# Performance work log

Hardware: AMD Instinct MI355X
Metric: run time of the kernel (lower is better)

Reference implementation:

```python
import jax, jax.numpy as jnp
import numpy as np

N_NODES = 50000
N_EDGES = 1600000
IN_C, HID_C, OUT_C = 256, 256, 10


def setup_inputs() -> dict:
    key = jax.random.key(0)
    ks = jax.random.split(key, 8)
    x = jax.random.normal(ks[0], (N_NODES, IN_C), dtype=jnp.float32)
    edge_index = jax.random.randint(ks[1], (2, N_EDGES), 0, N_NODES, dtype=jnp.int64)
    s1 = 1.0 / np.sqrt(IN_C)
    s2 = 1.0 / np.sqrt(HID_C)
    W1l = jax.random.normal(ks[2], (IN_C, HID_C), dtype=jnp.float32) * s1
    W1r = jax.random.normal(ks[3], (IN_C, HID_C), dtype=jnp.float32) * s1
    b1 = jnp.zeros((HID_C,), dtype=jnp.float32)
    W2l = jax.random.normal(ks[4], (HID_C, OUT_C), dtype=jnp.float32) * s2
    W2r = jax.random.normal(ks[5], (HID_C, OUT_C), dtype=jnp.float32) * s2
    b2 = jnp.zeros((OUT_C,), dtype=jnp.float32)
    return {"x": x, "edge_index": edge_index, "W1l": W1l, "W1r": W1r,
            "b1": b1, "W2l": W2l, "W2r": W2r, "b2": b2}


def _mean_agg(x, src, dst, n):
    # scatter-mean of source features into destination nodes
    summed = jax.ops.segment_sum(x[src], dst, num_segments=n)  # [N, C]
    cnt = jax.ops.segment_sum(jnp.ones_like(dst, dtype=x.dtype), dst, num_segments=n)
    return summed / jnp.maximum(cnt, 1.0)[:, None]


def _sage_conv(x, src, dst, Wl, Wr, b):
    # PyG SAGEConv (mean aggr): lin_l(mean_j x_j) + lin_r(x_i) + bias
    n = x.shape[0]
    agg = _mean_agg(x, src, dst, n)
    return agg @ Wl + x @ Wr + b


def reference(x, edge_index, W1l, W1r, b1, W2l, W2r, b2):
    src = edge_index[0]
    dst = edge_index[1]
    h = _sage_conv(x, src, dst, W1l, W1r, b1)
    h = jax.nn.relu(h)  # dropout skipped: eval mode
    out = _sage_conv(h, src, dst, W2l, W2r, b2)
    return jax.nn.log_softmax(out, axis=1)
```

## Files before the change

kernel.cpp:

```cpp
#include <hip/hip_runtime.h>
#include <hip/hip_bf16.h>

#define N_NODES 50000
#define N_EDGES 1600000
#define IN_C 256
#define HID_C 256
#define OUT_C 10
#define SLOT_CAP 96
#define NBUCKET 196
#define EBUF_CAP 9216
#define M_TILES 391
#define PART_BLOCKS 391
#define PREP_BLOCKS 532

typedef short bf16x8 __attribute__((ext_vector_type(8)));
typedef float f32x4 __attribute__((ext_vector_type(4)));

static __device__ __forceinline__ float b2f(short v) {
    unsigned u = (unsigned)(unsigned short)v << 16;
    return __builtin_bit_cast(float, u);
}
static __device__ __forceinline__ short f2b(float f) {
    __hip_bfloat16 h = __float2bfloat16(f);
    return __builtin_bit_cast(short, h);
}
static __device__ __forceinline__ int4 pack8i(float4 a, float4 b) {
    bf16x8 o;
    o[0] = f2b(a.x); o[1] = f2b(a.y); o[2] = f2b(a.z); o[3] = f2b(a.w);
    o[4] = f2b(b.x); o[5] = f2b(b.y); o[6] = f2b(b.z); o[7] = f2b(b.w);
    return __builtin_bit_cast(int4, o);
}

__global__ __launch_bounds__(256) void k_pp(
        const float* __restrict__ W1l, const float* __restrict__ W1r,
        const float* __restrict__ W2l, const float* __restrict__ W2r,
        __hip_bfloat16* __restrict__ Wt, float* __restrict__ Wt2f,
        const int* __restrict__ src, const int* __restrict__ dst,
        int* __restrict__ g_cursor, int* __restrict__ ebuf) {
    __shared__ int pbuf[3 * 256];
    int tid = threadIdx.x;
    int bid = blockIdx.x;

    if (bid < 512) {
        int idx = bid * 256 + tid;
        int n = idx >> 8, k = idx & 255;
        float v = (n < HID_C) ? W1l[k * HID_C + n] : W1r[k * HID_C + (n - HID_C)];
        Wt[idx] = __float2bfloat16(v);
        return;
    }
    if (bid < PREP_BLOCKS) {
        int idx = (bid - 512) * 256 + tid;
        int r = idx >> 8, k = idx & 255;
        if (r < OUT_C) Wt2f[r * 256 + k] = W2l[k * OUT_C + r];
        else           Wt2f[(16 + r - OUT_C) * 256 + k] = W2r[k * OUT_C + (r - OUT_C)];
        return;
    }

    int* hist = pbuf;
    int* base = pbuf + 256;
    int* pos  = pbuf + 512;
    int pb = bid - PREP_BLOCKS;
    if (tid < NBUCKET) { hist[tid] = 0; pos[tid] = 0; }
    __syncthreads();

    int4 s[4], d[4];
    bool valid[4];
#pragma unroll
    for (int q = 0; q < 4; ++q) {
        int idx = pb * 1024 + q * 256 + tid;
        valid[q] = (idx < N_EDGES / 4);
        if (valid[q]) {
            s[q] = ((const int4*)src)[idx];
            d[q] = ((const int4*)dst)[idx];
        }
    }
#pragma unroll
    for (int q = 0; q < 4; ++q) {
        if (valid[q]) {
            atomicAdd(&hist[d[q].x >> 8], 1);
            atomicAdd(&hist[d[q].y >> 8], 1);
            atomicAdd(&hist[d[q].z >> 8], 1);
            atomicAdd(&hist[d[q].w >> 8], 1);
        }
    }
    __syncthreads();
    if (tid < NBUCKET && hist[tid] > 0)
        base[tid] = atomicAdd(&g_cursor[tid], hist[tid]);
    __syncthreads();
#pragma unroll
    for (int q = 0; q < 4; ++q) {
        if (valid[q]) {
            int ss[4] = { s[q].x, s[q].y, s[q].z, s[q].w };
            int dd[4] = { d[q].x, d[q].y, d[q].z, d[q].w };
#pragma unroll
            for (int e = 0; e < 4; ++e) {
                int b = dd[e] >> 8;
                int p = base[b] + atomicAdd(&pos[b], 1);
                if (p < EBUF_CAP)
                    ebuf[b * EBUF_CAP + p] = ss[e] | ((dd[e] & 255) << 16);
            }
        }
    }
}

__global__ __launch_bounds__(256) void k_gb(
        const int* __restrict__ ebuf, const int* __restrict__ g_cursor,
        int* __restrict__ cnt, unsigned short* __restrict__ slots,
        const float* __restrict__ X, const __hip_bfloat16* __restrict__ Wt,
        const float* __restrict__ b1,
        __hip_bfloat16* __restrict__ Ab, __hip_bfloat16* __restrict__ Bh) {
    __shared__ short Smem[2 * 128 * 64];
    int tid = threadIdx.x;

    if (blockIdx.x < NBUCKET) {
        int* lcnt = (int*)Smem;
        int b = blockIdx.x;
        lcnt[tid] = 0;
        __syncthreads();
        int n_e = g_cursor[b];
        if (n_e > EBUF_CAP) n_e = EBUF_CAP;
        const int* eb = ebuf + b * EBUF_CAP;
        int n4 = n_e >> 2;
        for (int t = tid; t < n4; t += 256) {
            int4 v = ((const int4*)eb)[t];
            int vv[4] = { v.x, v.y, v.z, v.w };
#pragma unroll
            for (int e = 0; e < 4; ++e) {
                int dl = (vv[e] >> 16) & 255;
                int sv = vv[e] & 0xFFFF;
                int p = atomicAdd(&lcnt[dl], 1);
                if (p < SLOT_CAP) slots[(size_t)(b * 256 + dl) * SLOT_CAP + p] = (unsigned short)sv;
            }
        }
        for (int t = (n4 << 2) + tid; t < n_e; t += 256) {
            int vv = eb[t];
            int dl = (vv >> 16) & 255;
            int sv = vv & 0xFFFF;
            int p = atomicAdd(&lcnt[dl], 1);
            if (p < SLOT_CAP) slots[(size_t)(b * 256 + dl) * SLOT_CAP + p] = (unsigned short)sv;
        }
        __syncthreads();
        int nid = b * 256 + tid;
        if (nid < N_NODES) cnt[nid] = lcnt[tid];
        return;
    }

    short* As = Smem;
    short* Bs = Smem + 128 * 64;
    int fid = blockIdx.x - NBUCKET;
    int xcd = fid & 7, slot = fid >> 3;
    int m_t = (slot >> 2) * 8 + xcd;
    if (m_t >= M_TILES) return;
    int n_t = slot & 3;
    int m_base = m_t * 128;
    int n_base = n_t * 128;

    int wave = tid >> 6, lane = tid & 63;
    int r = lane & 15, quad = lane >> 4;
    int wr = wave >> 1, wc = wave & 1;

    int srow = tid >> 3;
    int kb8  = (tid & 7) * 16;
    int kelem = (tid & 7) * 8;
    int swz  = kb8 ^ ((srow & 7) << 4);

    f32x4 acc[4][4];
#pragma unroll
    for (int i = 0; i < 4; ++i)
#pragma unroll
        for (int j = 0; j < 4; ++j) acc[i][j] = f32x4{0.f, 0.f, 0.f, 0.f};

    int4 av[4], bv[4];
#pragma unroll
    for (int q = 0; q < 4; ++q) {
        int grow = m_base + q * 32 + srow;
        if (grow > N_NODES - 1) grow = N_NODES - 1;
        const float* xp = X + (size_t)grow * IN_C + kelem;
        av[q] = pack8i(*(const float4*)xp, *(const float4*)(xp + 4));
        int brow = n_base + q * 32 + srow;
        bv[q] = *(const int4*)((const char*)Wt + ((size_t)brow * 512 + kb8));
    }

    for (int kk = 0; kk < 4; ++kk) {
        if (kk) __syncthreads();
#pragma unroll
        for (int q = 0; q < 4; ++q) {
            *(int4*)((char*)As + (size_t)((q * 32 + srow) * 128 + swz)) = av[q];
            *(int4*)((char*)Bs + (size_t)((q * 32 + srow) * 128 + swz)) = bv[q];
        }
        __syncthreads();

        if (kk < 3) {
            int ke = (kk + 1) * 64 + kelem;
            int kbyte = (kk + 1) * 128 + kb8;
#pragma unroll
            for (int q = 0; q < 4; ++q) {
                int grow = m_base + q * 32 + srow;
                if (grow > N_NODES - 1) grow = N_NODES - 1;
                const float* xp = X + (size_t)grow * IN_C + ke;
                av[q] = pack8i(*(const float4*)xp, *(const float4*)(xp + 4));
                int brow = n_base + q * 32 + srow;
                bv[q] = *(const int4*)((const char*)Wt + ((size_t)brow * 512 + kbyte));
            }
        }

#pragma unroll
        for (int s = 0; s < 2; ++s) {
            int kfb = (s * 64 + quad * 16) ^ ((r & 7) << 4);
            bf16x8 a[4], b[4];
#pragma unroll
            for (int i = 0; i < 4; ++i)
                a[i] = *(const bf16x8*)((const char*)As + (size_t)((wr * 64 + i * 16 + r) * 128) + kfb);
#pragma unroll
            for (int j = 0; j < 4; ++j)
                b[j] = *(const bf16x8*)((const char*)Bs + (size_t)((wc * 64 + j * 16 + r) * 128) + kfb);
#pragma unroll
            for (int i = 0; i < 4; ++i)
#pragma unroll
                for (int j = 0; j < 4; ++j)
                    acc[i][j] = __builtin_amdgcn_mfma_f32_16x16x32_bf16(a[i], b[j], acc[i][j], 0, 0, 0);
        }
    }

    __syncthreads();
    short* Cs = Smem;
    bool left = (n_base < HID_C);
#pragma unroll
    for (int j = 0; j < 4; ++j) {
        int coll = wc * 64 + 16 * j + r;
        float bias = left ? 0.f : b1[n_base + coll - HID_C];
#pragma unroll
        for (int i = 0; i < 4; ++i) {
#pragma unroll
            for (int ii = 0; ii < 4; ++ii) {
                int rowl = wr * 64 + 16 * i + quad * 4 + ii;
                int byteoff = (coll * 2) ^ ((rowl & 7) << 4);
                *(short*)((char*)Cs + rowl * 256 + byteoff) = f2b(acc[i][j][ii] + bias);
            }
        }
    }
    __syncthreads();

    int rrow = tid >> 4;
    int cchunk = (tid & 15) * 16;
    size_t colbyte = left ? (size_t)(n_base * 2) : (size_t)((n_base - HID_C) * 2);
    char* outp = left ? (char*)Ab : (char*)Bh;
    for (int rb = 0; rb < 128; rb += 16) {
        int rowl = rb + rrow;
        int4 v = *(const int4*)((const char*)Cs + rowl * 256 + (cchunk ^ ((rowl & 7) << 4)));
        int grow = m_base + rowl;
        if (grow < N_NODES)
            *(int4*)(outp + (size_t)grow * 512 + colbyte + cchunk) = v;
    }
}

__global__ __launch_bounds__(256) void k_agg1f(
        const __hip_bfloat16* __restrict__ Ab, const __hip_bfloat16* __restrict__ Bh,
        const int* __restrict__ cnt, const unsigned short* __restrict__ slots,
        const float* __restrict__ Wt2f, const float* __restrict__ b2,
        float* __restrict__ CDl, float* __restrict__ CDr) {
    int wave = threadIdx.x >> 6, lane = threadIdx.x & 63;
    int nid = blockIdx.x * 4 + wave;
    int half = lane >> 5;
    int c8 = (lane & 31) * 8;
    const unsigned short* row = slots + (size_t)nid * SLOT_CAP;
    int n = cnt[nid];
    if (n > SLOT_CAP) n = SLOT_CAP;
    int mid = (n + 1) >> 1;
    int beg = half ? mid : 0;
    int end = half ? n : mid;

    float s0[8], s1[8], s2[8], s3[8];
#pragma unroll
    for (int j = 0; j < 8; ++j) { s0[j] = 0.f; s1[j] = 0.f; s2[j] = 0.f; s3[j] = 0.f; }

    const __hip_bfloat16* abc = Ab + c8;
    int e = beg;
    for (; e + 4 <= end; e += 4) {
        int i0 = row[e], i1 = row[e + 1], i2 = row[e + 2], i3 = row[e + 3];
        bf16x8 v0 = *(const bf16x8*)(abc + (size_t)i0 * HID_C);
        bf16x8 v1 = *(const bf16x8*)(abc + (size_t)i1 * HID_C);
        bf16x8 v2 = *(const bf16x8*)(abc + (size_t)i2 * HID_C);
        bf16x8 v3 = *(const bf16x8*)(abc + (size_t)i3 * HID_C);
#pragma unroll
        for (int j = 0; j < 8; ++j) {
            s0[j] += b2f(v0[j]); s1[j] += b2f(v1[j]);
            s2[j] += b2f(v2[j]); s3[j] += b2f(v3[j]);
        }
    }
    for (; e < end; ++e) {
        int i0 = row[e];
        bf16x8 v0 = *(const bf16x8*)(abc + (size_t)i0 * HID_C);
#pragma unroll
        for (int j = 0; j < 8; ++j) s0[j] += b2f(v0[j]);
    }
#pragma unroll
    for (int j = 0; j < 8; ++j) s0[j] += (s1[j] + s2[j]) + s3[j];
#pragma unroll
    for (int j = 0; j < 8; ++j) s0[j] += __shfl_down(s0[j], 32, 64);

    float h[8];
    float inv = 1.f / fmaxf((float)n, 1.f);
    if (half == 0) {
        bf16x8 bb = *(const bf16x8*)(Bh + (size_t)nid * HID_C + c8);
#pragma unroll
        for (int j = 0; j < 8; ++j)
            h[j] = fmaxf(s0[j] * inv + b2f(bb[j]), 0.f);
    }
#pragma unroll
    for (int j = 0; j < 8; ++j) h[j] = __shfl(h[j], lane & 31, 64);

    const float* wbase = Wt2f + (half ? 16 * 256 : 0);
    float acc[10];
#pragma unroll
    for (int j = 0; j < 10; ++j) {
        f32x4 w0 = *(const f32x4*)(wbase + j * 256 + c8);
        f32x4 w1 = *(const f32x4*)(wbase + j * 256 + c8 + 4);
        float a = h[0] * w0[0] + h[1] * w0[1] + h[2] * w0[2] + h[3] * w0[3]
                + h[4] * w1[0] + h[5] * w1[1] + h[6] * w1[2] + h[7] * w1[3];
#pragma unroll
        for (int off = 16; off > 0; off >>= 1)
            a += __shfl_down(a, off, 32);
        acc[j] = a;
    }
    if ((lane & 31) == 0) {
        if (half == 0) {
            float* o = CDl + (size_t)nid * 12;
#pragma unroll
            for (int j = 0; j < 10; ++j) o[j] = acc[j];
            o[10] = 0.f; o[11] = 0.f;
        } else {
            float* o = CDr + (size_t)nid * 12;
#pragma unroll
            for (int j = 0; j < 10; ++j) o[j] = acc[j] + b2[j];
        }
    }
}

__global__ __launch_bounds__(256) void k_agg2(
        const float* __restrict__ CDl, const float* __restrict__ CDr,
        const int* __restrict__ cnt, const unsigned short* __restrict__ slots,
        float* __restrict__ out) {
    int wave = threadIdx.x >> 6, lane = threadIdx.x & 63;
    int half = lane >> 5, sub = lane & 31;
    int nid = blockIdx.x * 8 + wave * 2 + half;
    const unsigned short* row = slots + (size_t)nid * SLOT_CAP;
    int n = cnt[nid];
    if (n > SLOT_CAP) n = SLOT_CAP;
    float s[10];
#pragma unroll
    for (int j = 0; j < 10; ++j) s[j] = 0.f;
    for (int e = sub; e < n; e += 32) {
        const float* cr = CDl + (size_t)row[e] * 12;
        f32x4 v0 = *(const f32x4*)cr;
        f32x4 v1 = *(const f32x4*)(cr + 4);
        f32x4 v2 = *(const f32x4*)(cr + 8);
#pragma unroll
        for (int j = 0; j < 4; ++j) { s[j] += v0[j]; s[4 + j] += v1[j]; }
        s[8] += v2[0]; s[9] += v2[1];
    }
#pragma unroll
    for (int j = 0; j < 10; ++j)
#pragma unroll
        for (int off = 16; off > 0; off >>= 1)
            s[j] += __shfl_down(s[j], off, 32);
    if (sub == 0) {
        float inv = 1.f / fmaxf((float)n, 1.f);
        const float* rr = CDr + (size_t)nid * 12;
        float z[10], mx = -1e30f;
#pragma unroll
        for (int j = 0; j < 10; ++j) {
            z[j] = s[j] * inv + rr[j];
            mx = fmaxf(mx, z[j]);
        }
        float se = 0.f;
#pragma unroll
        for (int j = 0; j < 10; ++j) se += expf(z[j] - mx);
        float lse = logf(se) + mx;
#pragma unroll
        for (int j = 0; j < 10; ++j) out[(size_t)nid * OUT_C + j] = z[j] - lse;
    }
}

extern "C" void kernel_launch(void* const* d_in, const int* in_sizes, int n_in,
                              void* d_out, int out_size, void* d_ws, size_t ws_size,
                              hipStream_t stream) {
    const float* x   = (const float*)d_in[0];
    const int*   ei  = (const int*)d_in[1];
    const float* W1l = (const float*)d_in[2];
    const float* W1r = (const float*)d_in[3];
    const float* b1  = (const float*)d_in[4];
    const float* W2l = (const float*)d_in[5];
    const float* W2r = (const float*)d_in[6];
    const float* b2  = (const float*)d_in[7];
    float* out = (float*)d_out;
    const int* src = ei;
    const int* dst = ei + N_EDGES;

    char* w = (char*)d_ws;
    size_t off = 0;
    auto alloc = [&](size_t bytes) -> void* {
        void* p = w + off;
        off = (off + bytes + 255) & ~(size_t)255;
        return p;
    };
    __hip_bfloat16* Wt   = (__hip_bfloat16*)alloc((size_t)2 * HID_C * IN_C * 2);
    float*          Wt2f = (float*)alloc((size_t)32 * 256 * 4);
    __hip_bfloat16* Ab   = (__hip_bfloat16*)alloc((size_t)N_NODES * HID_C * 2);
    __hip_bfloat16* Bh   = (__hip_bfloat16*)alloc((size_t)N_NODES * HID_C * 2);
    float* CDl = (float*)alloc((size_t)N_NODES * 12 * 4);
    float* CDr = (float*)alloc((size_t)N_NODES * 12 * 4);
    int* cnt      = (int*)alloc((size_t)N_NODES * 4);
    unsigned short* slots = (unsigned short*)alloc((size_t)N_NODES * SLOT_CAP * 2);
    int* g_cursor = (int*)alloc((size_t)NBUCKET * 4);
    int* ebuf     = (int*)alloc((size_t)NBUCKET * EBUF_CAP * 4);

    (void)hipMemsetAsync(g_cursor, 0, (size_t)NBUCKET * 4, stream);

    k_pp<<<PREP_BLOCKS + PART_BLOCKS, 256, 0, stream>>>(W1l, W1r, W2l, W2r, Wt, Wt2f,
                                                        src, dst, g_cursor, ebuf);
    k_gb<<<NBUCKET + 8 * 196, 256, 0, stream>>>(ebuf, g_cursor, cnt, slots,
                                                x, Wt, b1, Ab, Bh);
    k_agg1f<<<N_NODES / 4, 256, 0, stream>>>(Ab, Bh, cnt, slots, Wt2f, b2, CDl, CDr);
    k_agg2<<<N_NODES / 8, 256, 0, stream>>>(CDl, CDr, cnt, slots, out);
}
```

Before: 313.3 us.

## Fuse edge partitioning with GEMM kernel using per-block buckets and spin-wait flag

Moves edge partitioning out of the weight-prep kernel and into the GEMM kernel. Each partition block now writes to private per-(block,bucket) buffers, which removes the global histogram and cursor atomics and the memset. The bucket-gather blocks, placed last in the grid, spin on a completion counter before reading, so partitioning can overlap with the layer-1 GEMM. In exchange, each bucket gather walks 391 small sub-lists serially per thread. The spin-wait assumes all partition blocks get scheduled before the waiting blocks, which is a forward-progress risk.

```diff
diff --git a/kernel.cpp b/kernel.cpp
--- a/kernel.cpp
+++ b/kernel.cpp
@@ -8,10 +8,11 @@
 #define OUT_C 10
 #define SLOT_CAP 96
 #define NBUCKET 196
-#define EBUF_CAP 9216
+#define CAP2 56
 #define M_TILES 391
 #define PART_BLOCKS 391
-#define PREP_BLOCKS 532
+#define GEMM_BLOCKS 1568
+#define PREP_BLOCKS 533
 
 typedef short bf16x8 __attribute__((ext_vector_type(8)));
 typedef float f32x4 __attribute__((ext_vector_type(4)));
@@ -31,80 +32,30 @@
     return __builtin_bit_cast(int4, o);
 }
 
-__global__ __launch_bounds__(256) void k_pp(
-        const float* __restrict__ W1l, const float* __restrict__ W1r,
-        const float* __restrict__ W2l, const float* __restrict__ W2r,
-        __hip_bfloat16* __restrict__ Wt, float* __restrict__ Wt2f,
-        const int* __restrict__ src, const int* __restrict__ dst,
-        int* __restrict__ g_cursor, int* __restrict__ ebuf) {
-    __shared__ int pbuf[3 * 256];
-    int tid = threadIdx.x;
+__global__ void k_prep(const float* __restrict__ W1l, const float* __restrict__ W1r,
+                       const float* __restrict__ W2l, const float* __restrict__ W2r,
+                       __hip_bfloat16* __restrict__ Wt, float* __restrict__ Wt2f,
+                       int* __restrict__ part_done) {
     int bid = blockIdx.x;
-
     if (bid < 512) {
-        int idx = bid * 256 + tid;
+        int idx = bid * 256 + threadIdx.x;
         int n = idx >> 8, k = idx & 255;
         float v = (n < HID_C) ? W1l[k * HID_C + n] : W1r[k * HID_C + (n - HID_C)];
         Wt[idx] = __float2bfloat16(v);
-        return;
-    }
-    if (bid < PREP_BLOCKS) {
-        int idx = (bid - 512) * 256 + tid;
+    } else if (bid < 532) {
+        int idx = (bid - 512) * 256 + threadIdx.x;
         int r = idx >> 8, k = idx & 255;
         if (r < OUT_C) Wt2f[r * 256 + k] = W2l[k * OUT_C + r];
         else           Wt2f[(16 + r - OUT_C) * 256 + k] = W2r[k * OUT_C + (r - OUT_C)];
-        return;
-    }
-
-    int* hist = pbuf;
-    int* base = pbuf + 256;
-    int* pos  = pbuf + 512;
-    int pb = bid - PREP_BLOCKS;
-    if (tid < NBUCKET) { hist[tid] = 0; pos[tid] = 0; }
-    __syncthreads();
-
-    int4 s[4], d[4];
-    bool valid[4];
-#pragma unroll
-    for (int q = 0; q < 4; ++q) {
-        int idx = pb * 1024 + q * 256 + tid;
-        valid[q] = (idx < N_EDGES / 4);
-        if (valid[q]) {
-            s[q] = ((const int4*)src)[idx];
-            d[q] = ((const int4*)dst)[idx];
-        }
-    }
-#pragma unroll
-    for (int q = 0; q < 4; ++q) {
-        if (valid[q]) {
-            atomicAdd(&hist[d[q].x >> 8], 1);
-            atomicAdd(&hist[d[q].y >> 8], 1);
-            atomicAdd(&hist[d[q].z >> 8], 1);
-            atomicAdd(&hist[d[q].w >> 8], 1);
-        }
-    }
-    __syncthreads();
-    if (tid < NBUCKET && hist[tid] > 0)
-        base[tid] = atomicAdd(&g_cursor[tid], hist[tid]);
-    __syncthreads();
-#pragma unroll
-    for (int q = 0; q < 4; ++q) {
-        if (valid[q]) {
-            int ss[4] = { s[q].x, s[q].y, s[q].z, s[q].w };
-            int dd[4] = { d[q].x, d[q].y, d[q].z, d[q].w };
-#pragma unroll
-            for (int e = 0; e < 4; ++e) {
-                int b = dd[e] >> 8;
-                int p = base[b] + atomicAdd(&pos[b], 1);
-                if (p < EBUF_CAP)
-                    ebuf[b * EBUF_CAP + p] = ss[e] | ((dd[e] & 255) << 16);
-            }
-        }
-    }
-}
-
-__global__ __launch_bounds__(256) void k_gb(
-        const int* __restrict__ ebuf, const int* __restrict__ g_cursor,
+    } else {
+        if (threadIdx.x == 0) *part_done = 0;
+    }
+}
+
+__global__ __launch_bounds__(256) void k_gpb(
+        const int* __restrict__ src, const int* __restrict__ dst,
+        int* __restrict__ part_done, int* __restrict__ ebuf2,
+        unsigned char* __restrict__ cnt2,
         int* __restrict__ cnt, unsigned short* __restrict__ slots,
         const float* __restrict__ X, const __hip_bfloat16* __restrict__ Wt,
         const float* __restrict__ b1,
@@ -112,32 +63,72 @@
     __shared__ short Smem[2 * 128 * 64];
     int tid = threadIdx.x;
 
-    if (blockIdx.x < NBUCKET) {
+    if (blockIdx.x < PART_BLOCKS) {
+        int* pos = (int*)Smem;
+        int pb = blockIdx.x;
+        if (tid < NBUCKET) pos[tid] = 0;
+        __syncthreads();
+
+        int4 s[4], d[4];
+        bool valid[4];
+#pragma unroll
+        for (int q = 0; q < 4; ++q) {
+            int idx = pb * 1024 + q * 256 + tid;
+            valid[q] = (idx < N_EDGES / 4);
+            if (valid[q]) {
+                s[q] = ((const int4*)src)[idx];
+                d[q] = ((const int4*)dst)[idx];
+            }
+        }
+#pragma unroll
+        for (int q = 0; q < 4; ++q) {
+            if (valid[q]) {
+                int ss[4] = { s[q].x, s[q].y, s[q].z, s[q].w };
+                int dd[4] = { d[q].x, d[q].y, d[q].z, d[q].w };
+#pragma unroll
+                for (int e = 0; e < 4; ++e) {
+                    int b = dd[e] >> 8;
+                    int p = atomicAdd(&pos[b], 1);
+                    if (p < CAP2)
+                        ebuf2[((size_t)pb * NBUCKET + b) * CAP2 + p] =
+                            ss[e] | ((dd[e] & 255) << 16);
+                }
+            }
+        }
+        __syncthreads();
+        if (tid < NBUCKET) {
+            int c = pos[tid];
+            cnt2[(size_t)pb * NBUCKET + tid] = (unsigned char)(c > CAP2 ? CAP2 : c);
+        }
+        __syncthreads();
+        if (tid == 0)
+            __hip_atomic_fetch_add(part_done, 1, __ATOMIC_RELEASE, __HIP_MEMORY_SCOPE_AGENT);
+        return;
+    }
+
+    if (blockIdx.x >= PART_BLOCKS + GEMM_BLOCKS) {
+        if (tid == 0) {
+            while (__hip_atomic_load(part_done, __ATOMIC_RELAXED,
+                                     __HIP_MEMORY_SCOPE_AGENT) < PART_BLOCKS)
+                __builtin_amdgcn_s_sleep(8);
+        }
+        __syncthreads();
+        asm volatile("" ::: "memory");
+
         int* lcnt = (int*)Smem;
-        int b = blockIdx.x;
+        int b = blockIdx.x - PART_BLOCKS - GEMM_BLOCKS;
         lcnt[tid] = 0;
         __syncthreads();
-        int n_e = g_cursor[b];
-        if (n_e > EBUF_CAP) n_e = EBUF_CAP;
-        const int* eb = ebuf + b * EBUF_CAP;
-        int n4 = n_e >> 2;
-        for (int t = tid; t < n4; t += 256) {
-            int4 v = ((const int4*)eb)[t];
-            int vv[4] = { v.x, v.y, v.z, v.w };
-#pragma unroll
-            for (int e = 0; e < 4; ++e) {
-                int dl = (vv[e] >> 16) & 255;
-                int sv = vv[e] & 0xFFFF;
+        for (int blk = tid; blk < PART_BLOCKS; blk += 256) {
+            int len = cnt2[(size_t)blk * NBUCKET + b];
+            const int* base2 = ebuf2 + ((size_t)blk * NBUCKET + b) * CAP2;
+            for (int i = 0; i < len; ++i) {
+                int rec = base2[i];
+                int dl = (rec >> 16) & 255;
                 int p = atomicAdd(&lcnt[dl], 1);
-                if (p < SLOT_CAP) slots[(size_t)(b * 256 + dl) * SLOT_CAP + p] = (unsigned short)sv;
+                if (p < SLOT_CAP)
+                    slots[(size_t)(b * 256 + dl) * SLOT_CAP + p] = (unsigned short)(rec & 0xFFFF);
             }
-        }
-        for (int t = (n4 << 2) + tid; t < n_e; t += 256) {
-            int vv = eb[t];
-            int dl = (vv >> 16) & 255;
-            int sv = vv & 0xFFFF;
-            int p = atomicAdd(&lcnt[dl], 1);
-            if (p < SLOT_CAP) slots[(size_t)(b * 256 + dl) * SLOT_CAP + p] = (unsigned short)sv;
         }
         __syncthreads();
         int nid = b * 256 + tid;
@@ -147,7 +138,7 @@
 
     short* As = Smem;
     short* Bs = Smem + 128 * 64;
-    int fid = blockIdx.x - NBUCKET;
+    int fid = blockIdx.x - PART_BLOCKS;
     int xcd = fid & 7, slot = fid >> 3;
     int m_t = (slot >> 2) * 8 + xcd;
     if (m_t >= M_TILES) return;
@@ -412,15 +403,13 @@
     float* CDr = (float*)alloc((size_t)N_NODES * 12 * 4);
     int* cnt      = (int*)alloc((size_t)N_NODES * 4);
     unsigned short* slots = (unsigned short*)alloc((size_t)N_NODES * SLOT_CAP * 2);
-    int* g_cursor = (int*)alloc((size_t)NBUCKET * 4);
-    int* ebuf     = (int*)alloc((size_t)NBUCKET * EBUF_CAP * 4);
-
-    (void)hipMemsetAsync(g_cursor, 0, (size_t)NBUCKET * 4, stream);
-
-    k_pp<<<PREP_BLOCKS + PART_BLOCKS, 256, 0, stream>>>(W1l, W1r, W2l, W2r, Wt, Wt2f,
-                                                        src, dst, g_cursor, ebuf);
-    k_gb<<<NBUCKET + 8 * 196, 256, 0, stream>>>(ebuf, g_cursor, cnt, slots,
-                                                x, Wt, b1, Ab, Bh);
+    int* part_done = (int*)alloc(4);
+    int* ebuf2     = (int*)alloc((size_t)PART_BLOCKS * NBUCKET * CAP2 * 4);
+    unsigned char* cnt2 = (unsigned char*)alloc((size_t)PART_BLOCKS * NBUCKET);
+
+    k_prep<<<PREP_BLOCKS, 256, 0, stream>>>(W1l, W1r, W2l, W2r, Wt, Wt2f, part_done);
+    k_gpb<<<PART_BLOCKS + GEMM_BLOCKS + NBUCKET, 256, 0, stream>>>(
+        src, dst, part_done, ebuf2, cnt2, cnt, slots, x, Wt, b1, Ab, Bh);
     k_agg1f<<<N_NODES / 4, 256, 0, stream>>>(Ab, Bh, cnt, slots, Wt2f, b2, CDl, CDr);
     k_agg2<<<N_NODES / 8, 256, 0, stream>>>(CDl, CDr, cnt, slots, out);
 }
```

Result: slower. 339.6 us (+8.4%).
